# Optimization experiments

Measured on AMD Instinct MI355X. Metric: run time of the kernel, lower is better.

Reference implementation:

```python
import jax, jax.numpy as jnp
import numpy as np

TAO = 24
M = 7


def setup_inputs() -> dict:
    key = jax.random.key(0)
    k1, k2, k3 = jax.random.split(key, 3)
    B, S, C = 32, 2048, 7
    d_model = 512
    cm = C * (M + 1)  # 56 conv input channels
    x = jax.random.normal(k1, (B, S, C), dtype=jnp.float32)
    # total_conv: Conv1d(in=cm, out=d_model, kernel=3), kaiming_normal fan_in, leaky_relu
    fan_in = cm * 3
    gain = float(np.sqrt(2.0 / (1.0 + 0.01 ** 2)))
    std = gain / float(np.sqrt(fan_in))
    W = jax.random.normal(k2, (d_model, cm, 3), dtype=jnp.float32) * std
    bound = 1.0 / float(np.sqrt(fan_in))
    b = jax.random.uniform(k3, (d_model,), dtype=jnp.float32, minval=-bound, maxval=bound)
    return {"x": x, "W": W, "b": b}


def reference(x, W, b):
    B, S, C = x.shape
    mt = M * TAO  # delay-embedding lookback = 168
    n_valid = S - mt
    # sliding delay-embedding gather: for t in [mt, S), take x[t - k*tao] for k=0..M
    t_idx = jnp.arange(mt, S)                       # [n_valid]
    offs = jnp.arange(M + 1) * TAO                  # [M+1]
    tidx = t_idx[:, None] - offs[None, :]           # [n_valid, M+1]
    ext = x[:, tidx, :]                             # [B, n_valid, M+1, C]
    # torch reshape order: (n_valid, C, M+1) -> C major, offset minor
    fv = jnp.transpose(ext, (0, 1, 3, 2)).reshape(B, n_valid, C * (M + 1))
    # left-pad time axis with zeros to restore seq_len
    fv = jnp.pad(fv, ((0, 0), (mt, 0), (0, 0)))     # [B, S, C*(M+1)]
    # circular Conv1d (kernel 3, pad 1 circular)
    z = jnp.transpose(fv, (0, 2, 1))                # [B, C*(M+1), S]
    zp = jnp.pad(z, ((0, 0), (0, 0), (1, 1)), mode="wrap")
    out = jax.lax.conv_general_dilated(
        zp, W, window_strides=(1,), padding="VALID",
        dimension_numbers=("NCH", "OIH", "NCH"))    # [B, d_model, S]
    out = out + b[None, :, None]
    return jnp.transpose(out, (0, 2, 1))            # [B, S, d_model]
```

## Files before the change

kernel.cpp:

```cpp
#include <hip/hip_runtime.h>
#include <hip/hip_bf16.h>
#include <stdint.h>


#define TAO    24
#define MTAPS  7
#define C_IN   7
#define SEQ    2048
#define DMODEL 512
#define KP     72
#define RB     144
#define NROWS  65536
#define BM     128
#define BN     64
#define AROWS  130
#define A_CHUNKS (AROWS * 9)
#define B_CHUNKS (3 * BN * 9)
#define BS_H_STRIDE (BN * RB)

typedef __attribute__((ext_vector_type(8))) short frag_ab;
typedef __attribute__((ext_vector_type(4))) float frag_cd;

__global__ __launch_bounds__(256)
void prep_kernel(const float* __restrict__ x, const float* __restrict__ W,
                 __hip_bfloat16* __restrict__ G, __hip_bfloat16* __restrict__ Wb2)
{
    const int tid = threadIdx.x;
    if (blockIdx.x < 256) {
        const int row = blockIdx.x * 256 + tid;
        const int b   = row >> 11;
        const int t   = row & (SEQ - 1);
        const float* xb = x + b * (SEQ * C_IN);

        union { __hip_bfloat16 h[KP]; int4 v[9]; } u;
#pragma unroll
        for (int j = 0; j < 9; j++) u.v[j] = (int4){0, 0, 0, 0};

        if (t >= MTAPS * TAO) {
#pragma unroll
            for (int m = 0; m < 8; m++) {
                const float* p = xb + (t - TAO * m) * C_IN;
#pragma unroll
                for (int c = 0; c < C_IN; c++)
                    u.h[c * 8 + m] = __float2bfloat16(p[c]);
            }
        }
        int4* dst = (int4*)((char*)G + (size_t)row * RB);
#pragma unroll
        for (int j = 0; j < 9; j++) dst[j] = u.v[j];
    } else {
        const int idx = (blockIdx.x - 256) * 256 + tid;
        const int h = idx / DMODEL;
        const int o = idx - h * DMODEL;

        union { __hip_bfloat16 s[KP]; int4 v[9]; } u;
#pragma unroll
        for (int j = 0; j < 9; j++) u.v[j] = (int4){0, 0, 0, 0};
#pragma unroll
        for (int cm = 0; cm < 56; cm++)
            u.s[cm] = __float2bfloat16(W[o * 168 + cm * 3 + h]);

        int4* dst = (int4*)((char*)Wb2 + (size_t)idx * RB);
#pragma unroll
        for (int j = 0; j < 9; j++) dst[j] = u.v[j];
    }
}

__global__ __launch_bounds__(256, 3)
void gemm_kernel(const __hip_bfloat16* __restrict__ G,
                 const __hip_bfloat16* __restrict__ Wb2,
                 const float* __restrict__ bias,
                 float* __restrict__ out)
{
    __shared__ __align__(16) char lds[AROWS * RB + 3 * BN * RB];
    char* As = lds;
    char* Bs = lds + AROWS * RB;

    const int tid = threadIdx.x;
    const int nb  = blockIdx.x & 7;
    const int mb  = blockIdx.x >> 3;
    const int b   = mb >> 4;
    const int t0  = (mb & 15) * BM;
    const int o0  = nb * BN;

    {
        const char* Gb = (const char*)G + (size_t)b * SEQ * RB;
        for (int q = tid; q < A_CHUNKS; q += 256) {
            const int row = q / 9;
            const int c16 = q - row * 9;
            const int srow = (t0 - 1 + row + SEQ) & (SEQ - 1);
            __builtin_amdgcn_global_load_lds(
                (const __attribute__((address_space(1))) uint32_t*)(Gb + (size_t)srow * RB + c16 * 16),
                (__attribute__((address_space(3))) uint32_t*)(As + q * 16), 16, 0, 0);
        }
    }
    {
        for (int q = tid; q < B_CHUNKS; q += 256) {
            const int h = q / (BN * 9);
            const int rem = q - h * (BN * 9);
            const char* src = (const char*)Wb2 + ((size_t)(h * DMODEL + o0)) * RB + rem * 16;
            __builtin_amdgcn_global_load_lds(
                (const __attribute__((address_space(1))) uint32_t*)src,
                (__attribute__((address_space(3))) uint32_t*)(Bs + q * 16), 16, 0, 0);
        }
    }

    const int wave = tid >> 6;
    const int lane = tid & 63;
    const int wm   = (wave >> 1) * 64;
    const int wn   = (wave & 1) * 32;
    const int l15  = lane & 15;
    const int quad = lane >> 4;

    float bv[2];
#pragma unroll
    for (int ni = 0; ni < 2; ni++)
        bv[ni] = bias[o0 + wn + ni * 16 + l15];

    __syncthreads();

    frag_cd acc[4][2];
#pragma unroll
    for (int i = 0; i < 4; i++)
#pragma unroll
        for (int j = 0; j < 2; j++)
            acc[i][j] = (frag_cd){0.f, 0.f, 0.f, 0.f};

#pragma unroll
    for (int h = 0; h < 3; h++) {
#pragma unroll
        for (int kc = 0; kc < 2; kc++) {
            const int kbyte = kc * 64 + quad * 16;
            frag_ab a[4], bf[2];
#pragma unroll
            for (int mi = 0; mi < 4; mi++)
                a[mi] = *(const frag_ab*)(As + (wm + mi * 16 + l15 + h) * RB + kbyte);
#pragma unroll
            for (int ni = 0; ni < 2; ni++)
                bf[ni] = *(const frag_ab*)(Bs + h * BS_H_STRIDE + (wn + ni * 16 + l15) * RB + kbyte);
#pragma unroll
            for (int mi = 0; mi < 4; mi++)
#pragma unroll
                for (int ni = 0; ni < 2; ni++)
                    acc[mi][ni] = __builtin_amdgcn_mfma_f32_16x16x32_bf16(
                        a[mi], bf[ni], acc[mi][ni], 0, 0, 0);
        }
    }

    const size_t row0 = (size_t)mb * BM;
#pragma unroll
    for (int ni = 0; ni < 2; ni++) {
        const int o = o0 + wn + ni * 16 + l15;
#pragma unroll
        for (int mi = 0; mi < 4; mi++) {
            const size_t rbase = row0 + wm + mi * 16 + quad * 4;
#pragma unroll
            for (int reg = 0; reg < 4; reg++) {
                out[(rbase + reg) * DMODEL + o] = acc[mi][ni][reg] + bv[ni];
            }
        }
    }
}

#define KDIM  168
#define KPAD  192
#define FLDK  200
__global__ __launch_bounds__(256, 1)
void fused_tokenconv_kernel(const float* __restrict__ x,
                            const float* __restrict__ W,
                            const float* __restrict__ bias,
                            float* __restrict__ out)
{
    __shared__ __hip_bfloat16 As[128][FLDK];
    __shared__ __hip_bfloat16 Bs[128][FLDK];
    const int tid = threadIdx.x;
    const int blk = blockIdx.x;
    const int nb  = blk & 3;
    const int mb  = blk >> 2;
    const int b   = mb >> 4;
    const int t0  = (mb & 15) * 128;
    const int o0  = nb * 128;
    const float* xb = x + b * (SEQ * C_IN);

    for (int idx = tid; idx < 128 * KPAD; idx += 256) {
        int o_l = idx / KPAD;
        int i   = idx - o_l * KPAD;
        float v = (i < KDIM) ? W[(o0 + o_l) * KDIM + i] : 0.0f;
        Bs[o_l][i] = __float2bfloat16(v);
    }
    for (int idx = tid; idx < 128 * KPAD; idx += 256) {
        int t_l = idx / KPAD;
        int i   = idx - t_l * KPAD;
        float v = 0.0f;
        if (i < KDIM) {
            int c = i / 24;
            int r = i - c * 24;
            int m = r / 3;
            int h = r - m * 3;
            int s = (t0 + t_l + h - 1 + SEQ) & (SEQ - 1);
            if (s >= MTAPS * TAO) v = xb[(s - TAO * m) * C_IN + c];
        }
        As[t_l][i] = __float2bfloat16(v);
    }
    __syncthreads();

    const int wave = tid >> 6;
    const int lane = tid & 63;
    const int wm   = (wave >> 1) * 64;
    const int wn   = (wave & 1) * 64;
    const int l15  = lane & 15;
    const int quad = lane >> 4;

    frag_cd acc[4][4];
#pragma unroll
    for (int i = 0; i < 4; i++)
#pragma unroll
        for (int j = 0; j < 4; j++)
            acc[i][j] = (frag_cd){0.f, 0.f, 0.f, 0.f};

#pragma unroll
    for (int kc = 0; kc < KPAD / 32; kc++) {
        const int kof = kc * 32 + quad * 8;
        frag_ab a[4], bf[4];
#pragma unroll
        for (int mi = 0; mi < 4; mi++)
            a[mi] = *(const frag_ab*)&As[wm + mi * 16 + l15][kof];
#pragma unroll
        for (int ni = 0; ni < 4; ni++)
            bf[ni] = *(const frag_ab*)&Bs[wn + ni * 16 + l15][kof];
#pragma unroll
        for (int mi = 0; mi < 4; mi++)
#pragma unroll
            for (int ni = 0; ni < 4; ni++)
                acc[mi][ni] = __builtin_amdgcn_mfma_f32_16x16x32_bf16(
                    a[mi], bf[ni], acc[mi][ni], 0, 0, 0);
    }
    float* outb = out + (size_t)b * SEQ * DMODEL;
#pragma unroll
    for (int ni = 0; ni < 4; ni++) {
        const int o  = o0 + wn + ni * 16 + l15;
        const float bvv = bias[o];
#pragma unroll
        for (int mi = 0; mi < 4; mi++) {
#pragma unroll
            for (int reg = 0; reg < 4; reg++) {
                const int t = t0 + wm + mi * 16 + quad * 4 + reg;
                outb[(size_t)t * DMODEL + o] = acc[mi][ni][reg] + bvv;
            }
        }
    }
}

extern "C" void kernel_launch(void* const* d_in, const int* in_sizes, int n_in,
                              void* d_out, int out_size, void* d_ws, size_t ws_size,
                              hipStream_t stream) {
    const float* x    = (const float*)d_in[0];
    const float* W    = (const float*)d_in[1];
    const float* bias = (const float*)d_in[2];
    float* out        = (float*)d_out;

    const size_t g_bytes = (size_t)NROWS * RB;
    const size_t w_bytes = (size_t)3 * DMODEL * RB;
    if (ws_size >= g_bytes + w_bytes) {
        __hip_bfloat16* G   = (__hip_bfloat16*)d_ws;
        __hip_bfloat16* Wb2 = (__hip_bfloat16*)((char*)d_ws + g_bytes);
        hipLaunchKernelGGL(prep_kernel, dim3(262), dim3(256), 0, stream, x, W, G, Wb2);
        hipLaunchKernelGGL(gemm_kernel, dim3((NROWS / BM) * (DMODEL / BN)), dim3(256), 0, stream,
                           G, Wb2, bias, out);
    } else {
        hipLaunchKernelGGL(fused_tokenconv_kernel, dim3(32 * 16 * 4), dim3(256), 0, stream,
                           x, W, bias, out);
    }
}
```

Baseline: 162.4 us.

## Pre-swizzle weights into MFMA fragment layout and read them directly from global

```diff
diff --git a/kernel.cpp b/kernel.cpp
--- a/kernel.cpp
+++ b/kernel.cpp
@@ -11,19 +11,17 @@
 #define KP     72
 #define RB     144
 #define NROWS  65536
-#define BM     128
-#define BN     64
+#define BO     128
+#define BT     128
 #define AROWS  130
 #define A_CHUNKS (AROWS * 9)
-#define B_CHUNKS (3 * BN * 9)
-#define BS_H_STRIDE (BN * RB)
 
 typedef __attribute__((ext_vector_type(8))) short frag_ab;
 typedef __attribute__((ext_vector_type(4))) float frag_cd;
 
 __global__ __launch_bounds__(256)
 void prep_kernel(const float* __restrict__ x, const float* __restrict__ W,
-                 __hip_bfloat16* __restrict__ G, __hip_bfloat16* __restrict__ Wb2)
+                 __hip_bfloat16* __restrict__ G, __hip_bfloat16* __restrict__ Wf)
 {
     const int tid = threadIdx.x;
     if (blockIdx.x < 256) {
@@ -49,39 +47,39 @@
 #pragma unroll
         for (int j = 0; j < 9; j++) dst[j] = u.v[j];
     } else {
-        const int idx = (blockIdx.x - 256) * 256 + tid;
-        const int h = idx / DMODEL;
-        const int o = idx - h * DMODEL;
-
-        union { __hip_bfloat16 s[KP]; int4 v[9]; } u;
-#pragma unroll
-        for (int j = 0; j < 9; j++) u.v[j] = (int4){0, 0, 0, 0};
-#pragma unroll
-        for (int cm = 0; cm < 56; cm++)
-            u.s[cm] = __float2bfloat16(W[o * 168 + cm * 3 + h]);
-
-        int4* dst = (int4*)((char*)Wb2 + (size_t)idx * RB);
-#pragma unroll
-        for (int j = 0; j < 9; j++) dst[j] = u.v[j];
+        const int idx  = (blockIdx.x - 256) * 256 + tid;
+        const int lane = idx & 63;
+        const int kc   = (idx >> 6) & 1;
+        const int oc   = (idx >> 7) & 31;
+        const int h    = idx >> 12;
+        const int o    = oc * 16 + (lane & 15);
+        const int kof  = kc * 32 + (lane >> 4) * 8;
+
+        union { __hip_bfloat16 s[8]; int4 v; } u;
+#pragma unroll
+        for (int j = 0; j < 8; j++) {
+            const int k = kof + j;
+            float v = (k < 56) ? W[o * 168 + k * 3 + h] : 0.0f;
+            u.s[j] = __float2bfloat16(v);
+        }
+        ((int4*)Wf)[idx] = u.v;
     }
 }
 
 __global__ __launch_bounds__(256, 3)
 void gemm_kernel(const __hip_bfloat16* __restrict__ G,
-                 const __hip_bfloat16* __restrict__ Wb2,
+                 const __hip_bfloat16* __restrict__ Wf,
                  const float* __restrict__ bias,
                  float* __restrict__ out)
 {
-    __shared__ __align__(16) char lds[AROWS * RB + 3 * BN * RB];
-    char* As = lds;
-    char* Bs = lds + AROWS * RB;
+    __shared__ __align__(16) char As[AROWS * RB];
 
     const int tid = threadIdx.x;
-    const int nb  = blockIdx.x & 7;
-    const int mb  = blockIdx.x >> 3;
+    const int bo  = blockIdx.x & 3;
+    const int mb  = blockIdx.x >> 2;
     const int b   = mb >> 4;
-    const int t0  = (mb & 15) * BM;
-    const int o0  = nb * BN;
+    const int t0  = (mb & 15) * BT;
+    const int o0  = bo * BO;
 
     {
         const char* Gb = (const char*)G + (size_t)b * SEQ * RB;
@@ -94,70 +92,65 @@
                 (__attribute__((address_space(3))) uint32_t*)(As + q * 16), 16, 0, 0);
         }
     }
-    {
-        for (int q = tid; q < B_CHUNKS; q += 256) {
-            const int h = q / (BN * 9);
-            const int rem = q - h * (BN * 9);
-            const char* src = (const char*)Wb2 + ((size_t)(h * DMODEL + o0)) * RB + rem * 16;
-            __builtin_amdgcn_global_load_lds(
-                (const __attribute__((address_space(1))) uint32_t*)src,
-                (__attribute__((address_space(3))) uint32_t*)(Bs + q * 16), 16, 0, 0);
-        }
-    }
 
     const int wave = tid >> 6;
     const int lane = tid & 63;
-    const int wm   = (wave >> 1) * 64;
-    const int wn   = (wave & 1) * 32;
+    const int wo   = (wave >> 1) * 64;
+    const int wt   = (wave & 1) * 64;
     const int l15  = lane & 15;
     const int quad = lane >> 4;
 
-    float bv[2];
-#pragma unroll
-    for (int ni = 0; ni < 2; ni++)
-        bv[ni] = bias[o0 + wn + ni * 16 + l15];
+    float4 bias4[4];
+#pragma unroll
+    for (int mi = 0; mi < 4; mi++)
+        bias4[mi] = *(const float4*)&bias[o0 + wo + mi * 16 + quad * 4];
+
+    frag_cd acc[4][4];
+#pragma unroll
+    for (int i = 0; i < 4; i++)
+#pragma unroll
+        for (int j = 0; j < 4; j++)
+            acc[i][j] = (frag_cd){0.f, 0.f, 0.f, 0.f};
 
     __syncthreads();
 
-    frag_cd acc[4][2];
-#pragma unroll
-    for (int i = 0; i < 4; i++)
-#pragma unroll
-        for (int j = 0; j < 2; j++)
-            acc[i][j] = (frag_cd){0.f, 0.f, 0.f, 0.f};
-
+    const int octile = bo * 8 + (wo >> 4);
 #pragma unroll
     for (int h = 0; h < 3; h++) {
 #pragma unroll
         for (int kc = 0; kc < 2; kc++) {
+            frag_ab wfr[4], gfr[4];
+#pragma unroll
+            for (int mi = 0; mi < 4; mi++) {
+                const int tile = (h * 32 + octile + mi) * 2 + kc;
+                wfr[mi] = *(const frag_ab*)((const char*)Wf + (size_t)tile * 1024 + lane * 16);
+            }
             const int kbyte = kc * 64 + quad * 16;
-            frag_ab a[4], bf[2];
+#pragma unroll
+            for (int ni = 0; ni < 4; ni++)
+                gfr[ni] = *(const frag_ab*)(As + (wt + ni * 16 + l15 + h) * RB + kbyte);
 #pragma unroll
             for (int mi = 0; mi < 4; mi++)
-                a[mi] = *(const frag_ab*)(As + (wm + mi * 16 + l15 + h) * RB + kbyte);
-#pragma unroll
-            for (int ni = 0; ni < 2; ni++)
-                bf[ni] = *(const frag_ab*)(Bs + h * BS_H_STRIDE + (wn + ni * 16 + l15) * RB + kbyte);
-#pragma unroll
-            for (int mi = 0; mi < 4; mi++)
-#pragma unroll
-                for (int ni = 0; ni < 2; ni++)
+#pragma unroll
+                for (int ni = 0; ni < 4; ni++)
                     acc[mi][ni] = __builtin_amdgcn_mfma_f32_16x16x32_bf16(
-                        a[mi], bf[ni], acc[mi][ni], 0, 0, 0);
-        }
-    }
-
-    const size_t row0 = (size_t)mb * BM;
-#pragma unroll
-    for (int ni = 0; ni < 2; ni++) {
-        const int o = o0 + wn + ni * 16 + l15;
+                        wfr[mi], gfr[ni], acc[mi][ni], 0, 0, 0);
+        }
+    }
+
+    const size_t rowbase = (size_t)b * SEQ + t0 + wt;
+#pragma unroll
+    for (int ni = 0; ni < 4; ni++) {
+        const size_t r = rowbase + ni * 16 + l15;
+        float* orow = out + r * DMODEL + o0 + wo + quad * 4;
 #pragma unroll
         for (int mi = 0; mi < 4; mi++) {
-            const size_t rbase = row0 + wm + mi * 16 + quad * 4;
-#pragma unroll
-            for (int reg = 0; reg < 4; reg++) {
-                out[(rbase + reg) * DMODEL + o] = acc[mi][ni][reg] + bv[ni];
-            }
+            float4 v;
+            v.x = acc[mi][ni][0] + bias4[mi].x;
+            v.y = acc[mi][ni][1] + bias4[mi].y;
+            v.z = acc[mi][ni][2] + bias4[mi].z;
+            v.w = acc[mi][ni][3] + bias4[mi].w;
+            *(float4*)(orow + mi * 16) = v;
         }
     }
 }
@@ -260,13 +253,13 @@
     float* out        = (float*)d_out;
 
     const size_t g_bytes = (size_t)NROWS * RB;
-    const size_t w_bytes = (size_t)3 * DMODEL * RB;
+    const size_t w_bytes = (size_t)12288 * 16;
     if (ws_size >= g_bytes + w_bytes) {
-        __hip_bfloat16* G   = (__hip_bfloat16*)d_ws;
-        __hip_bfloat16* Wb2 = (__hip_bfloat16*)((char*)d_ws + g_bytes);
-        hipLaunchKernelGGL(prep_kernel, dim3(262), dim3(256), 0, stream, x, W, G, Wb2);
-        hipLaunchKernelGGL(gemm_kernel, dim3((NROWS / BM) * (DMODEL / BN)), dim3(256), 0, stream,
-                           G, Wb2, bias, out);
+        __hip_bfloat16* G  = (__hip_bfloat16*)d_ws;
+        __hip_bfloat16* Wf = (__hip_bfloat16*)((char*)d_ws + g_bytes);
+        hipLaunchKernelGGL(prep_kernel, dim3(304), dim3(256), 0, stream, x, W, G, Wf);
+        hipLaunchKernelGGL(gemm_kernel, dim3((DMODEL / BO) * (NROWS / BT)), dim3(256), 0, stream,
+                           G, Wf, bias, out);
     } else {
         hipLaunchKernelGGL(fused_tokenconv_kernel, dim3(32 * 16 * 4), dim3(256), 0, stream,
                            x, W, bias, out);
```

New measurement: 158.4 us. 1.03x faster.
